# Optimization experiments

Measured on AMD Instinct MI355X. Metric: run time of the kernel, lower is better.

## Reference

```python
import jax, jax.numpy as jnp
import numpy as np

B, S, D, H = 4, 2048, 1024, 16
W = D // H  # head width = 64


def setup_inputs() -> dict:
    key = jax.random.key(0)
    ks = jax.random.split(key, 7)
    sc = 0.02
    return {
        "x": jax.random.normal(ks[0], (B, S, D), dtype=jnp.float32),
        "mask": jnp.ones((B, S), dtype=jnp.int32),
        "Wq": jax.random.normal(ks[1], (D, D), dtype=jnp.float32) * sc,
        "bq": jax.random.normal(ks[2], (D,), dtype=jnp.float32) * sc,
        "Wk": jax.random.normal(ks[3], (D, D), dtype=jnp.float32) * sc,
        "bk": jax.random.normal(ks[4], (D,), dtype=jnp.float32) * sc,
        "Wv": jax.random.normal(ks[5], (D, D), dtype=jnp.float32) * sc,
        "bv": jax.random.normal(ks[6], (D,), dtype=jnp.float32) * sc,
    }


def reference(x, mask, Wq, bq, Wk, bk, Wv, bv):
    # Linear projections (torch Linear: y = x @ W.T + b)
    q = x @ Wq.T + bq  # (B,S,D)
    k = x @ Wk.T + bk
    v = x @ Wv.T + bv
    # split D -> (H, W) and move heads forward: (B,H,S,W)
    def split(t):
        return t.reshape(B, S, H, W).transpose(0, 2, 1, 3)
    q, k, v = split(q), split(k), split(v)
    scale = 1.0 / np.sqrt(W).astype(np.float32)
    scores = jnp.einsum("bhsw,bhtw->bhst", q, k) * scale  # (B,H,S,S)
    m = mask[:, None, None, :].astype(scores.dtype)  # (B,1,1,S)
    scores = scores - 10000.0 * (1.0 - m)
    probs = jax.nn.softmax(scores, axis=-1)  # dropout p=0.0 -> identity
    h = jnp.einsum("bhst,bhtw->bhsw", probs, v)  # (B,H,S,W)
    h = h.transpose(0, 2, 1, 3).reshape(B, S, D)  # merge heads
    return h
```

## Files before the change

kernel.cpp:

```cpp
#include <hip/hip_runtime.h>
#include <hip/hip_bf16.h>


#define NB 4
#define NS 2048
#define ND 1024
#define NH 16
#define NW 64

typedef __bf16 bf16;
typedef __bf16 bf16x2 __attribute__((ext_vector_type(2)));
typedef __bf16 bf16x4 __attribute__((ext_vector_type(4)));
typedef __bf16 bf16x8 __attribute__((ext_vector_type(8)));
typedef float f32x4 __attribute__((ext_vector_type(4)));
typedef float f32x16 __attribute__((ext_vector_type(16)));
typedef unsigned u32x4 __attribute__((ext_vector_type(4)));

__device__ __forceinline__ void gld_lds16(const void* g, void* l) {
  __builtin_amdgcn_global_load_lds(
      (const __attribute__((address_space(1))) void*)g,
      (__attribute__((address_space(3))) void*)l, 16, 0, 0);
}

__device__ __forceinline__ unsigned pack2(float lo, float hi) {
  bf16x2 t;
  t[0] = (bf16)lo;
  t[1] = (bf16)hi;
  return __builtin_bit_cast(unsigned, t);
}

__global__ void cast_f32_bf16(const float* __restrict__ src,
                              bf16* __restrict__ dst, int n) {
  int i = (blockIdx.x * blockDim.x + threadIdx.x) * 8;
  int stride = gridDim.x * blockDim.x * 8;
  for (; i < n; i += stride) {
    float4 a = *reinterpret_cast<const float4*>(src + i);
    float4 b = *reinterpret_cast<const float4*>(src + i + 4);
    bf16x8 o;
    o[0] = (bf16)a.x; o[1] = (bf16)a.y; o[2] = (bf16)a.z; o[3] = (bf16)a.w;
    o[4] = (bf16)b.x; o[5] = (bf16)b.y; o[6] = (bf16)b.z; o[7] = (bf16)b.w;
    *reinterpret_cast<bf16x8*>(dst + i) = o;
  }
}

__global__ void cast_weights(const float* __restrict__ a,
                             const float* __restrict__ b,
                             const float* __restrict__ c,
                             bf16* __restrict__ dst) {
  const int n = ND * ND;
  const int which = blockIdx.y;
  const float* src = (which == 0) ? a : ((which == 1) ? b : c);
  bf16* d = dst + (size_t)which * n;
  int i = (blockIdx.x * blockDim.x + threadIdx.x) * 8;
  float4 u = *reinterpret_cast<const float4*>(src + i);
  float4 v = *reinterpret_cast<const float4*>(src + i + 4);
  bf16x8 o;
  o[0] = (bf16)u.x; o[1] = (bf16)u.y; o[2] = (bf16)u.z; o[3] = (bf16)u.w;
  o[4] = (bf16)v.x; o[5] = (bf16)v.y; o[6] = (bf16)v.z; o[7] = (bf16)v.w;
  *reinterpret_cast<bf16x8*>(d + i) = o;
}

__global__ void mask_to_bf16(const int* __restrict__ mask,
                             bf16* __restrict__ mb, int n) {
  int i = blockIdx.x * blockDim.x + threadIdx.x;
  if (i < n) mb[i] = (bf16)(mask[i] ? 1.0f : 0.0f);
}

__global__ __launch_bounds__(256) void proj_fused(
    const bf16* __restrict__ xb,
    const bf16* __restrict__ wall,
    const float* __restrict__ bq,
    const float* __restrict__ bk,
    const float* __restrict__ bv,
    const int* __restrict__ mask,
    bf16* __restrict__ qh,
    bf16* __restrict__ kh,
    bf16* __restrict__ vt) {
  const int mode = blockIdx.y;
  const bf16* wmat = wall + (size_t)mode * ND * ND;
  const float* bias = (mode == 0) ? bq : ((mode == 1) ? bk : bv);

  __shared__ alignas(16) bf16 a_lds[128][64];
  __shared__ alignas(16) bf16 b_lds[128][64];

  const int tid = threadIdx.x;
  const int wave = tid >> 6;
  const int lane = tid & 63;
  const int wr = wave >> 1, wc = wave & 1;

  const int p = blockIdx.x;
  const int xcd = p & 7, q = p >> 3;
  const int m0 = (xcd * 8 + (q & 7)) * 128;
  const int n0 = (q >> 3) * 128;

  f32x4 acc[4][4] = {};

  const int srow = tid >> 3;
  const int scol = (tid & 7) * 8;
  const int sw_scol = scol ^ ((srow & 7) << 3);
  const int xr = (lane & 7) << 3;
  const int lr = lane & 15;
  const int g = lane >> 4;
  const int kq = g * 8;

  for (int k0 = 0; k0 < 1024; k0 += 64) {
#pragma unroll
    for (int c = 0; c < 4; ++c) {
      const int row = srow + c * 32;
      gld_lds16(xb + (size_t)(m0 + row) * 1024 + k0 + sw_scol, &a_lds[row][scol]);
      gld_lds16(wmat + (size_t)(n0 + row) * 1024 + k0 + sw_scol, &b_lds[row][scol]);
    }
    __syncthreads();
#pragma unroll
    for (int kk = 0; kk < 64; kk += 32) {
      bf16x8 af[4], bfr[4];
      const int col = (kk + kq) ^ xr;
#pragma unroll
      for (int mf = 0; mf < 4; ++mf)
        af[mf] = *reinterpret_cast<const bf16x8*>(&a_lds[wr * 64 + mf * 16 + lr][col]);
#pragma unroll
      for (int nf = 0; nf < 4; ++nf)
        bfr[nf] = *reinterpret_cast<const bf16x8*>(&b_lds[wc * 64 + nf * 16 + lr][col]);
#pragma unroll
      for (int nf = 0; nf < 4; ++nf)
#pragma unroll
        for (int mf = 0; mf < 4; ++mf)
          acc[nf][mf] = __builtin_amdgcn_mfma_f32_16x16x32_bf16(bfr[nf], af[mf], acc[nf][mf], 0, 0, 0);
    }
    __syncthreads();
  }

  if (mode == 2) {
#pragma unroll
    for (int mf = 0; mf < 4; ++mf) {
      const int i = m0 + wr * 64 + mf * 16 + lr;
      const int b = i >> 11, s = i & 2047;
      const float mskv = mask[b * NS + s] ? 1.f : 0.f;
#pragma unroll
      for (int nf = 0; nf < 4; ++nf) {
        const int j0 = n0 + wc * 64 + nf * 16 + g * 4;
        const f32x4 bj = *reinterpret_cast<const f32x4*>(&bias[j0]);
        const int h = j0 >> 6, w0 = j0 & 63;
#pragma unroll
        for (int r = 0; r < 4; ++r)
          vt[((size_t)(b * NH + h) * NW + w0 + r) * NS + s] =
              (bf16)((acc[nf][mf][r] + bj[r]) * mskv);
      }
    }
  } else {
    bf16* dst = (mode == 0) ? qh : kh;
    const float scl = (mode == 0) ? 0.18033688011112042f : 1.0f;
#pragma unroll
    for (int nf = 0; nf < 4; ++nf) {
      const int j0 = n0 + wc * 64 + nf * 16 + g * 4;
      const f32x4 bj = *reinterpret_cast<const f32x4*>(&bias[j0]);
      const int h = j0 >> 6, w0 = j0 & 63;
#pragma unroll
      for (int mf = 0; mf < 4; ++mf) {
        const int i = m0 + wr * 64 + mf * 16 + lr;
        const int b = i >> 11, s = i & 2047;
        bf16x4 pk;
#pragma unroll
        for (int r = 0; r < 4; ++r)
          pk[r] = (bf16)((acc[nf][mf][r] + bj[r]) * scl);
        *reinterpret_cast<bf16x4*>(&dst[(((size_t)(b * NH + h)) * NS + s) * NW + w0]) = pk;
      }
    }
  }
}

__global__ __launch_bounds__(256, 4) void attn_kernel(
    const bf16* __restrict__ qh,
    const bf16* __restrict__ kh,
    const bf16* __restrict__ vt,
    const bf16* __restrict__ mb16,
    float* __restrict__ out) {
  __shared__ alignas(16) bf16 k_lds[2][64][64];
  __shared__ alignas(16) bf16 v_lds[2][64][64];

  const int tid = threadIdx.x;
  const int wave = tid >> 6;
  const int lane = tid & 63;
  const int lq = lane & 31;
  const int hi = lane >> 5;
  const int xr = (lq & 7) << 3;

  const int p = blockIdx.x;
  const int w_id = (p & 7) * 128 + (p >> 3);
  const int bh = w_id >> 4;
  const int b = bh >> 4;
  const int q0 = (w_id & 15) * 128;
  const size_t headoff = (size_t)bh * NS * NW;

  bf16x8 qf[4];
  {
    const bf16* qp = qh + headoff + (size_t)(q0 + wave * 32 + lq) * NW + hi * 8;
#pragma unroll
    for (int m = 0; m < 4; ++m)
      qf[m] = *reinterpret_cast<const bf16x8*>(qp + m * 16);
  }

  f32x16 o0 = {}, o1 = {}, lt = {};
  const bf16* mp = mb16 + b * NS;

  const int srow = tid >> 3;
  const int scol = (tid & 7) * 8;
  const int sw_scol = scol ^ ((srow & 7) << 3);

#define STAGE(buf, kt)                                                          \
  {                                                                             \
    _Pragma("unroll") for (int c = 0; c < 2; ++c) {                             \
      const int row = srow + c * 32;                                            \
      gld_lds16(kh + headoff + (size_t)((kt) + row) * NW + sw_scol,             \
                &k_lds[buf][row][scol]);                                        \
      gld_lds16(vt + headoff + (size_t)row * NS + (kt) + sw_scol,               \
                &v_lds[buf][row][scol]);                                        \
    }                                                                           \
  }

#define EXPPACK(S, PA0, PA1)                                                    \
  {                                                                             \
    unsigned w_[8];                                                             \
    _Pragma("unroll") for (int j = 0; j < 8; ++j)                               \
        w_[j] = pack2(__builtin_amdgcn_exp2f(S[2 * j]),                         \
                      __builtin_amdgcn_exp2f(S[2 * j + 1]));                    \
    asm("v_permlane32_swap_b32 %0, %1" : "+v"(w_[0]), "+v"(w_[2]));             \
    asm("v_permlane32_swap_b32 %0, %1" : "+v"(w_[1]), "+v"(w_[3]));             \
    asm("v_permlane32_swap_b32 %0, %1" : "+v"(w_[4]), "+v"(w_[6]));             \
    asm("v_permlane32_swap_b32 %0, %1" : "+v"(w_[5]), "+v"(w_[7]));             \
    u32x4 u0 = {w_[0], w_[1], w_[2], w_[3]};                                    \
    u32x4 u1 = {w_[4], w_[5], w_[6], w_[7]};                                    \
    PA0 = __builtin_bit_cast(bf16x8, u0);                                       \
    PA1 = __builtin_bit_cast(bf16x8, u1);                                       \
  }

  STAGE(0, 0);
  __syncthreads();

  int cur = 0;
  for (int kt = 0; kt < NS; kt += 64) {
    if (kt + 64 < NS) STAGE(cur ^ 1, kt + 64);

    f32x16 s0 = {}, s1 = {};
    __builtin_amdgcn_s_setprio(1);
#pragma unroll
    for (int m = 0; m < 4; ++m) {
      const int col = (m * 16 + hi * 8) ^ xr;
      bf16x8 kf0 = *reinterpret_cast<const bf16x8*>(&k_lds[cur][lq][col]);
      s0 = __builtin_amdgcn_mfma_f32_32x32x16_bf16(kf0, qf[m], s0, 0, 0, 0);
      bf16x8 kf1 = *reinterpret_cast<const bf16x8*>(&k_lds[cur][32 + lq][col]);
      s1 = __builtin_amdgcn_mfma_f32_32x32x16_bf16(kf1, qf[m], s1, 0, 0, 0);
    }
    __builtin_amdgcn_s_setprio(0);

    bf16x8 pa0, pa1, pa2, pa3;
    EXPPACK(s0, pa0, pa1);
    EXPPACK(s1, pa2, pa3);

    const bf16* mpk = mp + kt + hi * 8;
    bf16x8 mf00 = *reinterpret_cast<const bf16x8*>(mpk);
    bf16x8 mf01 = *reinterpret_cast<const bf16x8*>(mpk + 16);
    bf16x8 mf10 = *reinterpret_cast<const bf16x8*>(mpk + 32);
    bf16x8 mf11 = *reinterpret_cast<const bf16x8*>(mpk + 48);

    __builtin_amdgcn_s_setprio(1);
    lt = __builtin_amdgcn_mfma_f32_32x32x16_bf16(pa0, mf00, lt, 0, 0, 0);
    lt = __builtin_amdgcn_mfma_f32_32x32x16_bf16(pa1, mf01, lt, 0, 0, 0);
    lt = __builtin_amdgcn_mfma_f32_32x32x16_bf16(pa2, mf10, lt, 0, 0, 0);
    lt = __builtin_amdgcn_mfma_f32_32x32x16_bf16(pa3, mf11, lt, 0, 0, 0);
#pragma unroll
    for (int G = 0; G < 2; ++G) {
      const bf16x8 a0 = G ? pa2 : pa0;
      const bf16x8 a1 = G ? pa3 : pa1;
      const int c0 = (G * 32 + hi * 8) ^ xr;
      const int c1 = (G * 32 + 16 + hi * 8) ^ xr;
      bf16x8 v00 = *reinterpret_cast<const bf16x8*>(&v_lds[cur][lq][c0]);
      o0 = __builtin_amdgcn_mfma_f32_32x32x16_bf16(a0, v00, o0, 0, 0, 0);
      bf16x8 v01 = *reinterpret_cast<const bf16x8*>(&v_lds[cur][lq][c1]);
      o0 = __builtin_amdgcn_mfma_f32_32x32x16_bf16(a1, v01, o0, 0, 0, 0);
      bf16x8 v10 = *reinterpret_cast<const bf16x8*>(&v_lds[cur][32 + lq][c0]);
      o1 = __builtin_amdgcn_mfma_f32_32x32x16_bf16(a0, v10, o1, 0, 0, 0);
      bf16x8 v11 = *reinterpret_cast<const bf16x8*>(&v_lds[cur][32 + lq][c1]);
      o1 = __builtin_amdgcn_mfma_f32_32x32x16_bf16(a1, v11, o1, 0, 0, 0);
    }
    __builtin_amdgcn_s_setprio(0);

    __syncthreads();
    cur ^= 1;
  }

  const int h = bh & 15;
  float* op = out + ((size_t)b * NS) * ND + h * NW;
#pragma unroll
  for (int r = 0; r < 16; ++r) {
    const int sq = q0 + wave * 32 + (r & 3) + 8 * (r >> 2) + 4 * hi;
    const float inv = 1.0f / lt[r];
    op[(size_t)sq * ND + lq] = o0[r] * inv;
    op[(size_t)sq * ND + 32 + lq] = o1[r] * inv;
  }
#undef STAGE
#undef EXPPACK
}

extern "C" void kernel_launch(void* const* d_in, const int* in_sizes, int n_in,
                              void* d_out, int out_size, void* d_ws, size_t ws_size,
                              hipStream_t stream) {
  const float* x = (const float*)d_in[0];
  const int* mask = (const int*)d_in[1];
  const float* Wq = (const float*)d_in[2];
  const float* bq = (const float*)d_in[3];
  const float* Wk = (const float*)d_in[4];
  const float* bk = (const float*)d_in[5];
  const float* Wv = (const float*)d_in[6];
  const float* bv = (const float*)d_in[7];
  float* out = (float*)d_out;

  char* ws = (char*)d_ws;
  bf16* wall = (bf16*)(ws + (size_t)(0) * (1 << 20));
  bf16* qhb = (bf16*)(ws + (size_t)(6) * (1 << 20));
  bf16* khb = (bf16*)(ws + (size_t)(22) * (1 << 20));
  bf16* vtb = (bf16*)(ws + (size_t)(38) * (1 << 20));
  bf16* mb16 = (bf16*)(ws + (size_t)(54) * (1 << 20));
  bf16* xb = (bf16*)d_out;

  cast_f32_bf16<<<2048, 256, 0, stream>>>(x, xb, NB * NS * ND);
  cast_weights<<<dim3(512, 3), 256, 0, stream>>>(Wq, Wk, Wv, wall);
  mask_to_bf16<<<32, 256, 0, stream>>>(mask, mb16, NB * NS);
  proj_fused<<<dim3(512, 3), 256, 0, stream>>>(xb, wall, bq, bk, bv, mask,
                                               qhb, khb, vtb);
  attn_kernel<<<1024, 256, 0, stream>>>(qhb, khb, vtb, mb16, out);
}
```

Before: 253.9 us.

## Process two 128-row query tiles per attention block to reuse K/V tiles

Each attention block now covers 256 query rows, 128 per group across two register sets, instead of 128, which halves the grid to 512 blocks. Every K/V tile staged in LDS feeds twice as many MFMAs, so global and LDS traffic per unit of compute is halved. The cost is about double the accumulator registers, which the launch bound relaxed from 4 to 2 blocks per SM reflects, so occupancy and latency hiding drop.

```diff
diff --git a/kernel.cpp b/kernel.cpp
--- a/kernel.cpp
+++ b/kernel.cpp
@@ -169,7 +169,7 @@
   }
 }
 
-__global__ __launch_bounds__(256, 4) void attn_kernel(
+__global__ __launch_bounds__(256, 2) void attn_kernel(
     const bf16* __restrict__ qh,
     const bf16* __restrict__ kh,
     const bf16* __restrict__ vt,
@@ -186,21 +186,24 @@
   const int xr = (lq & 7) << 3;
 
   const int p = blockIdx.x;
-  const int w_id = (p & 7) * 128 + (p >> 3);
-  const int bh = w_id >> 4;
+  const int w_id = (p & 7) * 64 + (p >> 3);
+  const int bh = w_id >> 3;
   const int b = bh >> 4;
-  const int q0 = (w_id & 15) * 128;
+  const int q0 = (w_id & 7) * 256;
   const size_t headoff = (size_t)bh * NS * NW;
 
-  bf16x8 qf[4];
+  bf16x8 qfa[4], qfb[4];
   {
     const bf16* qp = qh + headoff + (size_t)(q0 + wave * 32 + lq) * NW + hi * 8;
 #pragma unroll
-    for (int m = 0; m < 4; ++m)
-      qf[m] = *reinterpret_cast<const bf16x8*>(qp + m * 16);
-  }
-
-  f32x16 o0 = {}, o1 = {}, lt = {};
+    for (int m = 0; m < 4; ++m) {
+      qfa[m] = *reinterpret_cast<const bf16x8*>(qp + m * 16);
+      qfb[m] = *reinterpret_cast<const bf16x8*>(qp + 128 * NW + m * 16);
+    }
+  }
+
+  f32x16 o0a = {}, o1a = {}, o0b = {}, o1b = {}, lta = {}, ltb = {};
+  const f32x16 kZ = {};
   const bf16* mp = mb16 + b * NS;
 
   const int srow = tid >> 3;
@@ -241,21 +244,25 @@
   for (int kt = 0; kt < NS; kt += 64) {
     if (kt + 64 < NS) STAGE(cur ^ 1, kt + 64);
 
-    f32x16 s0 = {}, s1 = {};
+    f32x16 s0a, s1a, s0b, s1b;
     __builtin_amdgcn_s_setprio(1);
 #pragma unroll
     for (int m = 0; m < 4; ++m) {
       const int col = (m * 16 + hi * 8) ^ xr;
       bf16x8 kf0 = *reinterpret_cast<const bf16x8*>(&k_lds[cur][lq][col]);
-      s0 = __builtin_amdgcn_mfma_f32_32x32x16_bf16(kf0, qf[m], s0, 0, 0, 0);
       bf16x8 kf1 = *reinterpret_cast<const bf16x8*>(&k_lds[cur][32 + lq][col]);
-      s1 = __builtin_amdgcn_mfma_f32_32x32x16_bf16(kf1, qf[m], s1, 0, 0, 0);
+      s0a = __builtin_amdgcn_mfma_f32_32x32x16_bf16(kf0, qfa[m], m ? s0a : kZ, 0, 0, 0);
+      s1a = __builtin_amdgcn_mfma_f32_32x32x16_bf16(kf1, qfa[m], m ? s1a : kZ, 0, 0, 0);
+      s0b = __builtin_amdgcn_mfma_f32_32x32x16_bf16(kf0, qfb[m], m ? s0b : kZ, 0, 0, 0);
+      s1b = __builtin_amdgcn_mfma_f32_32x32x16_bf16(kf1, qfb[m], m ? s1b : kZ, 0, 0, 0);
     }
     __builtin_amdgcn_s_setprio(0);
 
-    bf16x8 pa0, pa1, pa2, pa3;
-    EXPPACK(s0, pa0, pa1);
-    EXPPACK(s1, pa2, pa3);
+    bf16x8 pa0, pa1, pa2, pa3, pb0, pb1, pb2, pb3;
+    EXPPACK(s0a, pa0, pa1);
+    EXPPACK(s1a, pa2, pa3);
+    EXPPACK(s0b, pb0, pb1);
+    EXPPACK(s1b, pb2, pb3);
 
     const bf16* mpk = mp + kt + hi * 8;
     bf16x8 mf00 = *reinterpret_cast<const bf16x8*>(mpk);
@@ -264,24 +271,34 @@
     bf16x8 mf11 = *reinterpret_cast<const bf16x8*>(mpk + 48);
 
     __builtin_amdgcn_s_setprio(1);
-    lt = __builtin_amdgcn_mfma_f32_32x32x16_bf16(pa0, mf00, lt, 0, 0, 0);
-    lt = __builtin_amdgcn_mfma_f32_32x32x16_bf16(pa1, mf01, lt, 0, 0, 0);
-    lt = __builtin_amdgcn_mfma_f32_32x32x16_bf16(pa2, mf10, lt, 0, 0, 0);
-    lt = __builtin_amdgcn_mfma_f32_32x32x16_bf16(pa3, mf11, lt, 0, 0, 0);
+    lta = __builtin_amdgcn_mfma_f32_32x32x16_bf16(pa0, mf00, lta, 0, 0, 0);
+    lta = __builtin_amdgcn_mfma_f32_32x32x16_bf16(pa1, mf01, lta, 0, 0, 0);
+    lta = __builtin_amdgcn_mfma_f32_32x32x16_bf16(pa2, mf10, lta, 0, 0, 0);
+    lta = __builtin_amdgcn_mfma_f32_32x32x16_bf16(pa3, mf11, lta, 0, 0, 0);
+    ltb = __builtin_amdgcn_mfma_f32_32x32x16_bf16(pb0, mf00, ltb, 0, 0, 0);
+    ltb = __builtin_amdgcn_mfma_f32_32x32x16_bf16(pb1, mf01, ltb, 0, 0, 0);
+    ltb = __builtin_amdgcn_mfma_f32_32x32x16_bf16(pb2, mf10, ltb, 0, 0, 0);
+    ltb = __builtin_amdgcn_mfma_f32_32x32x16_bf16(pb3, mf11, ltb, 0, 0, 0);
 #pragma unroll
     for (int G = 0; G < 2; ++G) {
       const bf16x8 a0 = G ? pa2 : pa0;
       const bf16x8 a1 = G ? pa3 : pa1;
+      const bf16x8 b0 = G ? pb2 : pb0;
+      const bf16x8 b1 = G ? pb3 : pb1;
       const int c0 = (G * 32 + hi * 8) ^ xr;
       const int c1 = (G * 32 + 16 + hi * 8) ^ xr;
       bf16x8 v00 = *reinterpret_cast<const bf16x8*>(&v_lds[cur][lq][c0]);
-      o0 = __builtin_amdgcn_mfma_f32_32x32x16_bf16(a0, v00, o0, 0, 0, 0);
       bf16x8 v01 = *reinterpret_cast<const bf16x8*>(&v_lds[cur][lq][c1]);
-      o0 = __builtin_amdgcn_mfma_f32_32x32x16_bf16(a1, v01, o0, 0, 0, 0);
       bf16x8 v10 = *reinterpret_cast<const bf16x8*>(&v_lds[cur][32 + lq][c0]);
-      o1 = __builtin_amdgcn_mfma_f32_32x32x16_bf16(a0, v10, o1, 0, 0, 0);
       bf16x8 v11 = *reinterpret_cast<const bf16x8*>(&v_lds[cur][32 + lq][c1]);
-      o1 = __builtin_amdgcn_mfma_f32_32x32x16_bf16(a1, v11, o1, 0, 0, 0);
+      o0a = __builtin_amdgcn_mfma_f32_32x32x16_bf16(a0, v00, o0a, 0, 0, 0);
+      o0a = __builtin_amdgcn_mfma_f32_32x32x16_bf16(a1, v01, o0a, 0, 0, 0);
+      o1a = __builtin_amdgcn_mfma_f32_32x32x16_bf16(a0, v10, o1a, 0, 0, 0);
+      o1a = __builtin_amdgcn_mfma_f32_32x32x16_bf16(a1, v11, o1a, 0, 0, 0);
+      o0b = __builtin_amdgcn_mfma_f32_32x32x16_bf16(b0, v00, o0b, 0, 0, 0);
+      o0b = __builtin_amdgcn_mfma_f32_32x32x16_bf16(b1, v01, o0b, 0, 0, 0);
+      o1b = __builtin_amdgcn_mfma_f32_32x32x16_bf16(b0, v10, o1b, 0, 0, 0);
+      o1b = __builtin_amdgcn_mfma_f32_32x32x16_bf16(b1, v11, o1b, 0, 0, 0);
     }
     __builtin_amdgcn_s_setprio(0);
 
@@ -293,10 +310,15 @@
   float* op = out + ((size_t)b * NS) * ND + h * NW;
 #pragma unroll
   for (int r = 0; r < 16; ++r) {
-    const int sq = q0 + wave * 32 + (r & 3) + 8 * (r >> 2) + 4 * hi;
-    const float inv = 1.0f / lt[r];
-    op[(size_t)sq * ND + lq] = o0[r] * inv;
-    op[(size_t)sq * ND + 32 + lq] = o1[r] * inv;
+    const int rr = (r & 3) + 8 * (r >> 2) + 4 * hi;
+    const int sqa = q0 + wave * 32 + rr;
+    const int sqb = sqa + 128;
+    const float inva = 1.0f / lta[r];
+    const float invb = 1.0f / ltb[r];
+    op[(size_t)sqa * ND + lq] = o0a[r] * inva;
+    op[(size_t)sqa * ND + 32 + lq] = o1a[r] * inva;
+    op[(size_t)sqb * ND + lq] = o0b[r] * invb;
+    op[(size_t)sqb * ND + 32 + lq] = o1b[r] * invb;
   }
 #undef STAGE
 #undef EXPPACK
@@ -328,5 +350,5 @@
   mask_to_bf16<<<32, 256, 0, stream>>>(mask, mb16, NB * NS);
   proj_fused<<<dim3(512, 3), 256, 0, stream>>>(xb, wall, bq, bk, bv, mask,
                                                qhb, khb, vtb);
-  attn_kernel<<<1024, 256, 0, stream>>>(qhb, khb, vtb, mb16, out);
-}
+  attn_kernel<<<512, 256, 0, stream>>>(qhb, khb, vtb, mb16, out);
+}
```

Result: no change. 249.5 us (-1.7%).
